# Optimization experiments

Measured on AMD Instinct MI355X. Metric: run time of the kernel, lower is better.

## Reference

```python
import jax, jax.numpy as jnp
import numpy as np

SQRT_D_K = 64 ** 0.5  # d_model ** 0.5 from __init__
NEG_INF = -1e9


def setup_inputs() -> dict:
    key = jax.random.key(0)
    kq, kk, kv, kp = jax.random.split(key, 4)
    B, H, S, Dh = 4, 16, 2048, 64
    q = jax.random.normal(kq, (B, H, S, Dh), dtype=jnp.float32)
    k = jax.random.normal(kk, (B, H, S, Dh), dtype=jnp.float32)
    v = jax.random.normal(kv, (B, H, S, Dh), dtype=jnp.float32)
    # causal mask: 1 above the diagonal (positions to mask), [1,1,S,S]
    casual_mask = jnp.triu(jnp.ones((S, S), dtype=jnp.int32), k=1)[None, None]
    # padding mask: 1 marks padded tokens, [B,S]
    padding_mask = jax.random.randint(kp, (B, S), 0, 2, dtype=jnp.int32)
    return {"q": q, "k": k, "v": v, "casual_mask": casual_mask,
            "padding_mask": padding_mask}


def reference(q, k, v, casual_mask, padding_mask):
    # score: [B,H,S,S]
    score = jnp.einsum("bhqd,bhkd->bhqk", q, k) / SQRT_D_K
    score = jnp.where(casual_mask == 1, NEG_INF, score)
    score = jnp.where(padding_mask[:, None, None, :] == 1, NEG_INF, score)
    attn_weights = jax.nn.softmax(score, axis=-1)
    # dropout p=0.0 (eval) -> identity
    attention_output = jnp.einsum("bhqk,bhkd->bhqd", attn_weights, v)
    return attention_output, attn_weights
```

## Files before the change

kernel.cpp:

```cpp
#include <hip/hip_runtime.h>
#include <hip/hip_bf16.h>

#define S_LEN 2048
#define DH    64
#define QT    128
#define KT    64
#define NW    4

typedef __attribute__((ext_vector_type(8))) short bf16x8;
typedef __attribute__((ext_vector_type(4))) float f32x4;
typedef __attribute__((ext_vector_type(4))) unsigned u32x4;
typedef __attribute__((ext_vector_type(2))) unsigned u32x2;

static __device__ __forceinline__ unsigned cvtpk(float a, float b) {
    unsigned r;
    asm("v_cvt_pk_bf16_f32 %0, %1, %2" : "=v"(r) : "v"(a), "v"(b));
    return r;
}

__global__ __launch_bounds__(256) void attn_main(
    const float* __restrict__ Q, const float* __restrict__ K,
    const float* __restrict__ V, const int* __restrict__ PAD,
    float* __restrict__ OUT, float* __restrict__ W)
{
    __shared__ short Kt[KT][72];
    __shared__ short VT[DH][72];
    __shared__ short Pb[NW][16][72];
    __shared__ float sinv[2][NW][16];
    __shared__ unsigned long long padm[32];

    const int orig = blockIdx.x;
    const int wg   = (orig & 7) * 128 + (orig >> 3);
    const int bh   = wg >> 4;
    const int qt   = 15 - (wg & 15);
    const int b    = bh >> 4;
    const int q0   = qt * QT;

    const int tid  = threadIdx.x;
    const int wv   = tid >> 6;
    const int l    = tid & 63;
    const int lr   = l & 15;
    const int lg   = l >> 4;
    const int k2   = (tid & 31) * 2;
    const int dblk = (tid >> 5) * 8;

    const size_t hoff = (size_t)bh * S_LEN * DH;
    const float* Qh = Q + hoff;
    const float* Kh = K + hoff;
    const float* Vh = V + hoff;
    float* Oh = OUT + hoff;
    float* Wh = W + (size_t)bh * S_LEN * S_LEN;

    const int nkt    = 2 * qt + 2;
    const int ktmaxA = 2 * qt;

    for (int i = tid; i < S_LEN; i += 256) {
        unsigned long long m = __ballot(PAD[b * S_LEN + i] != 0);
        if (l == 0) padm[i >> 6] = m;
    }

    bf16x8 qfA[2], qfB[2];
    #pragma unroll
    for (int blk = 0; blk < 2; ++blk) {
        const float* qp = Qh + (size_t)(q0 + blk * 64 + wv * 16 + lr) * DH + lg * 8;
        #pragma unroll
        for (int h = 0; h < 2; ++h) {
            f32x4 a  = *reinterpret_cast<const f32x4*>(qp + h * 32);
            f32x4 b4 = *reinterpret_cast<const f32x4*>(qp + h * 32 + 4);
            u32x4 t;
            t[0] = cvtpk(a[0] * 0.125f,  a[1] * 0.125f);
            t[1] = cvtpk(a[2] * 0.125f,  a[3] * 0.125f);
            t[2] = cvtpk(b4[0] * 0.125f, b4[1] * 0.125f);
            t[3] = cvtpk(b4[2] * 0.125f, b4[3] * 0.125f);
            (blk ? qfB[h] : qfA[h]) = __builtin_bit_cast(bf16x8, t);
        }
    }

    const f32x4 z4 = {0.f, 0.f, 0.f, 0.f};
    f32x4 accA[4] = {z4, z4, z4, z4};
    f32x4 accB[4] = {z4, z4, z4, z4};
    float rsA = 0.f, rsB = 0.f;
    const int qcolA = q0 + wv * 16 + lr;
    const int qcolB = qcolA + 64;

    auto ablock = [&](const bf16x8 (&qf)[2], const int qcol, float& rsref,
                      f32x4 (&accb)[4], const unsigned long long pm, const int ktbase) {
        f32x4 sc[4] = {z4, z4, z4, z4};
        #pragma unroll
        for (int s = 0; s < 4; ++s)
            #pragma unroll
            for (int h = 0; h < 2; ++h) {
                bf16x8 kf = *reinterpret_cast<const bf16x8*>(&Kt[s * 16 + lr][h * 32 + lg * 8]);
                sc[s] = __builtin_amdgcn_mfma_f32_16x16x32_bf16(kf, qf[h], sc[s], 0, 0, 0);
            }
        #pragma unroll
        for (int s = 0; s < 4; ++s) {
            const int kbase = ktbase + s * 16 + lg * 4;
            float e[4];
            #pragma unroll
            for (int r = 0; r < 4; ++r) {
                const bool padded = (pm >> (s * 16 + lg * 4 + r)) & 1ull;
                const bool ok = (kbase + r <= qcol) && !padded;
                e[r] = ok ? __expf(sc[s][r]) : 0.f;
                rsref += e[r];
            }
            u32x2 p2 = { cvtpk(e[0], e[1]), cvtpk(e[2], e[3]) };
            *reinterpret_cast<u32x2*>(&Pb[wv][lr][s * 16 + lg * 4]) = p2;
        }
        #pragma unroll
        for (int kk = 0; kk < 2; ++kk) {
            bf16x8 pf = *reinterpret_cast<const bf16x8*>(&Pb[wv][lr][kk * 32 + lg * 8]);
            #pragma unroll
            for (int dt = 0; dt < 4; ++dt) {
                bf16x8 vf = *reinterpret_cast<const bf16x8*>(&VT[dt * 16 + lr][kk * 32 + lg * 8]);
                accb[dt] = __builtin_amdgcn_mfma_f32_16x16x32_bf16(pf, vf, accb[dt], 0, 0, 0);
            }
        }
    };

    for (int kt = 0; kt < nkt; ++kt) {
        __syncthreads();
        {
            const float* kp = Kh + ((size_t)(kt * KT) + l) * DH + wv * 16;
            f32x4 pk0 = *reinterpret_cast<const f32x4*>(kp);
            f32x4 pk1 = *reinterpret_cast<const f32x4*>(kp + 4);
            f32x4 pk2 = *reinterpret_cast<const f32x4*>(kp + 8);
            f32x4 pk3 = *reinterpret_cast<const f32x4*>(kp + 12);
            const float* vp = Vh + ((size_t)(kt * KT) + k2) * DH + dblk;
            f32x4 pva0 = *reinterpret_cast<const f32x4*>(vp);
            f32x4 pva1 = *reinterpret_cast<const f32x4*>(vp + 4);
            f32x4 pvb0 = *reinterpret_cast<const f32x4*>(vp + DH);
            f32x4 pvb1 = *reinterpret_cast<const f32x4*>(vp + DH + 4);
            u32x4 ta, tb;
            ta[0] = cvtpk(pk0[0], pk0[1]); ta[1] = cvtpk(pk0[2], pk0[3]);
            ta[2] = cvtpk(pk1[0], pk1[1]); ta[3] = cvtpk(pk1[2], pk1[3]);
            tb[0] = cvtpk(pk2[0], pk2[1]); tb[1] = cvtpk(pk2[2], pk2[3]);
            tb[2] = cvtpk(pk3[0], pk3[1]); tb[3] = cvtpk(pk3[2], pk3[3]);
            *reinterpret_cast<u32x4*>(&Kt[l][wv * 16])     = ta;
            *reinterpret_cast<u32x4*>(&Kt[l][wv * 16 + 8]) = tb;
            #pragma unroll
            for (int j = 0; j < 4; ++j)
                *reinterpret_cast<unsigned*>(&VT[dblk + j][k2])     = cvtpk(pva0[j], pvb0[j]);
            #pragma unroll
            for (int j = 0; j < 4; ++j)
                *reinterpret_cast<unsigned*>(&VT[dblk + 4 + j][k2]) = cvtpk(pva1[j], pvb1[j]);
        }
        __syncthreads();

        const unsigned long long pm = padm[kt];
        if (kt <= ktmaxA) ablock(qfA, qcolA, rsA, accA, pm, kt * KT);
        ablock(qfB, qcolB, rsB, accB, pm, kt * KT);
    }

    rsA += __shfl_xor(rsA, 16, 64); rsA += __shfl_xor(rsA, 32, 64);
    rsB += __shfl_xor(rsB, 16, 64); rsB += __shfl_xor(rsB, 32, 64);
    const float invA = rsA > 0.f ? 1.f / rsA : 0.f;
    const float invB = rsB > 0.f ? 1.f / rsB : 0.f;

    if (lg == 0) { sinv[0][wv][lr] = invA; sinv[1][wv][lr] = invB; }
    float inv4A[4], inv4B[4];
    #pragma unroll
    for (int r = 0; r < 4; ++r) {
        inv4A[r] = sinv[0][wv][lg * 4 + r];
        inv4B[r] = sinv[1][wv][lg * 4 + r];
    }

    const int qa = q0 + wv * 16 + lg * 4;
    #pragma unroll
    for (int dt = 0; dt < 4; ++dt)
        #pragma unroll
        for (int r = 0; r < 4; ++r) {
            Oh[(size_t)(qa + r) * DH + dt * 16 + lr]      = accA[dt][r] * inv4A[r];
            Oh[(size_t)(qa + 64 + r) * DH + dt * 16 + lr] = accB[dt][r] * inv4B[r];
        }

    auto wblock = [&](const bf16x8 (&qf)[2], const int qcol, const float inv,
                      const unsigned long long pm, const int ktbase) {
        f32x4 sc[4] = {z4, z4, z4, z4};
        #pragma unroll
        for (int s = 0; s < 4; ++s)
            #pragma unroll
            for (int h = 0; h < 2; ++h) {
                bf16x8 kf = *reinterpret_cast<const bf16x8*>(&Kt[s * 16 + lr][h * 32 + lg * 8]);
                sc[s] = __builtin_amdgcn_mfma_f32_16x16x32_bf16(kf, qf[h], sc[s], 0, 0, 0);
            }
        #pragma unroll
        for (int s = 0; s < 4; ++s) {
            const int kbase = ktbase + s * 16 + lg * 4;
            f32x4 t;
            #pragma unroll
            for (int r = 0; r < 4; ++r) {
                const bool padded = (pm >> (s * 16 + lg * 4 + r)) & 1ull;
                const bool ok = (kbase + r <= qcol) && !padded;
                t[r] = ok ? __expf(sc[s][r]) * inv : 0.f;
            }
            __builtin_nontemporal_store(t,
                reinterpret_cast<f32x4*>(Wh + (size_t)qcol * S_LEN + kbase));
        }
    };

    for (int kt = 0; kt < nkt; ++kt) {
        __syncthreads();
        {
            const float* kp = Kh + ((size_t)(kt * KT) + l) * DH + wv * 16;
            f32x4 pk0 = *reinterpret_cast<const f32x4*>(kp);
            f32x4 pk1 = *reinterpret_cast<const f32x4*>(kp + 4);
            f32x4 pk2 = *reinterpret_cast<const f32x4*>(kp + 8);
            f32x4 pk3 = *reinterpret_cast<const f32x4*>(kp + 12);
            u32x4 ta, tb;
            ta[0] = cvtpk(pk0[0], pk0[1]); ta[1] = cvtpk(pk0[2], pk0[3]);
            ta[2] = cvtpk(pk1[0], pk1[1]); ta[3] = cvtpk(pk1[2], pk1[3]);
            tb[0] = cvtpk(pk2[0], pk2[1]); tb[1] = cvtpk(pk2[2], pk2[3]);
            tb[2] = cvtpk(pk3[0], pk3[1]); tb[3] = cvtpk(pk3[2], pk3[3]);
            *reinterpret_cast<u32x4*>(&Kt[l][wv * 16])     = ta;
            *reinterpret_cast<u32x4*>(&Kt[l][wv * 16 + 8]) = tb;
        }
        __syncthreads();

        const unsigned long long pm = padm[kt];
        if (kt <= ktmaxA) wblock(qfA, qcolA, invA, pm, kt * KT);
        wblock(qfB, qcolB, invB, pm, kt * KT);
    }

    {
        #pragma unroll 1
        for (int row = 0; row < QT; ++row) {
            const int kend = q0 + (row < 64 ? 64 : 128);
            const int n4 = (S_LEN - kend) >> 2;
            f32x4* dst = reinterpret_cast<f32x4*>(Wh + (size_t)(q0 + row) * S_LEN + kend);
            for (int i = tid; i < n4; i += 256)
                __builtin_nontemporal_store(z4, dst + i);
        }
    }
}

__global__ __launch_bounds__(256) void attn_fixup(
    const int* __restrict__ PAD, const float* __restrict__ V,
    float* __restrict__ OUT, float* __restrict__ W)
{
    const int bh = blockIdx.x;
    const int b  = bh >> 4;
    const int tid = threadIdx.x;
    __shared__ int red;
    __shared__ float tmp[256];
    __shared__ float vs[DH];
    if (tid == 0) red = S_LEN;
    __syncthreads();
    int m = S_LEN;
    for (int i = tid; i < S_LEN; i += 256)
        if (PAD[b * S_LEN + i] == 0) m = min(m, i);
    atomicMin(&red, m);
    __syncthreads();
    const int fz = red;
    if (fz == 0) return;

    const float* Vh = V + (size_t)bh * S_LEN * DH;
    float a = 0.f;
    const int dcol = tid & 63, part = tid >> 6;
    for (int kk = part; kk < S_LEN; kk += 4) a += Vh[(size_t)kk * DH + dcol];
    tmp[tid] = a;
    __syncthreads();
    if (tid < DH)
        vs[tid] = (tmp[tid] + tmp[tid + 64] + tmp[tid + 128] + tmp[tid + 192]) * (1.f / S_LEN);
    __syncthreads();

    float* Wh = W + (size_t)bh * S_LEN * S_LEN;
    float* Oh = OUT + (size_t)bh * S_LEN * DH;
    const f32x4 u = {1.f / S_LEN, 1.f / S_LEN, 1.f / S_LEN, 1.f / S_LEN};
    for (int qa2 = 0; qa2 < fz; ++qa2) {
        f32x4* dst = reinterpret_cast<f32x4*>(Wh + (size_t)qa2 * S_LEN);
        for (int i = tid; i < S_LEN / 4; i += 256) dst[i] = u;
        if (tid < DH) Oh[(size_t)qa2 * DH + tid] = vs[tid];
    }
}

extern "C" void kernel_launch(void* const* d_in, const int* in_sizes, int n_in,
                              void* d_out, int out_size, void* d_ws, size_t ws_size,
                              hipStream_t stream) {
    const float* q   = (const float*)d_in[0];
    const float* k   = (const float*)d_in[1];
    const float* v   = (const float*)d_in[2];
    const int*   pad = (const int*)d_in[4];

    float* out = (float*)d_out;
    float* w   = out + (size_t)4 * 16 * S_LEN * DH;

    attn_main<<<dim3(64 * 16), dim3(256), 0, stream>>>(q, k, v, pad, out, w);
    attn_fixup<<<dim3(64), dim3(256), 0, stream>>>(pad, v, out, w);
}
```

Baseline: 472.7 us.

## Double-buffer K tiles in LDS for the attention-weights pass with register prefetch

The weights-writing loop now prefetches the next K tile from global memory into registers before computing the current tile. After the current tile's MFMAs and stores, it converts and stores the prefetched tile into the alternate LDS buffer, reusing the VT buffer. This replaces two syncthreads per iteration with one barrier and hides global load latency behind compute. The trade-off is extra register pressure, and the code relies on VT being free and the same shape during this phase.

```diff
diff --git a/kernel.cpp b/kernel.cpp
--- a/kernel.cpp
+++ b/kernel.cpp
@@ -174,14 +174,24 @@
             Oh[(size_t)(qa + 64 + r) * DH + dt * 16 + lr] = accB[dt][r] * inv4B[r];
         }
 
-    auto wblock = [&](const bf16x8 (&qf)[2], const int qcol, const float inv,
+    auto stK = [&](short (*KB)[72], const f32x4& a0, const f32x4& a1,
+                   const f32x4& a2, const f32x4& a3) {
+        u32x4 ta, tb;
+        ta[0] = cvtpk(a0[0], a0[1]); ta[1] = cvtpk(a0[2], a0[3]);
+        ta[2] = cvtpk(a1[0], a1[1]); ta[3] = cvtpk(a1[2], a1[3]);
+        tb[0] = cvtpk(a2[0], a2[1]); tb[1] = cvtpk(a2[2], a2[3]);
+        tb[2] = cvtpk(a3[0], a3[1]); tb[3] = cvtpk(a3[2], a3[3]);
+        *reinterpret_cast<u32x4*>(&KB[l][wv * 16])     = ta;
+        *reinterpret_cast<u32x4*>(&KB[l][wv * 16 + 8]) = tb;
+    };
+    auto wblock = [&](short (*KB)[72], const bf16x8 (&qf)[2], const int qcol, const float inv,
                       const unsigned long long pm, const int ktbase) {
         f32x4 sc[4] = {z4, z4, z4, z4};
         #pragma unroll
         for (int s = 0; s < 4; ++s)
             #pragma unroll
             for (int h = 0; h < 2; ++h) {
-                bf16x8 kf = *reinterpret_cast<const bf16x8*>(&Kt[s * 16 + lr][h * 32 + lg * 8]);
+                bf16x8 kf = *reinterpret_cast<const bf16x8*>(&KB[s * 16 + lr][h * 32 + lg * 8]);
                 sc[s] = __builtin_amdgcn_mfma_f32_16x16x32_bf16(kf, qf[h], sc[s], 0, 0, 0);
             }
         #pragma unroll
@@ -199,27 +209,44 @@
         }
     };
 
+    short (*kbuf0)[72] = Kt;
+    short (*kbuf1)[72] = VT;
+
+    __syncthreads();
+    {
+        const float* kp = Kh + (size_t)l * DH + wv * 16;
+        f32x4 a0 = *reinterpret_cast<const f32x4*>(kp);
+        f32x4 a1 = *reinterpret_cast<const f32x4*>(kp + 4);
+        f32x4 a2 = *reinterpret_cast<const f32x4*>(kp + 8);
+        f32x4 a3 = *reinterpret_cast<const f32x4*>(kp + 12);
+        stK(kbuf0, a0, a1, a2, a3);
+    }
+    asm volatile("s_waitcnt lgkmcnt(0)" ::: "memory");
+    __builtin_amdgcn_sched_barrier(0);
+    __builtin_amdgcn_s_barrier();
+    __builtin_amdgcn_sched_barrier(0);
+
+    int cur = 0;
     for (int kt = 0; kt < nkt; ++kt) {
-        __syncthreads();
-        {
-            const float* kp = Kh + ((size_t)(kt * KT) + l) * DH + wv * 16;
-            f32x4 pk0 = *reinterpret_cast<const f32x4*>(kp);
-            f32x4 pk1 = *reinterpret_cast<const f32x4*>(kp + 4);
-            f32x4 pk2 = *reinterpret_cast<const f32x4*>(kp + 8);
-            f32x4 pk3 = *reinterpret_cast<const f32x4*>(kp + 12);
-            u32x4 ta, tb;
-            ta[0] = cvtpk(pk0[0], pk0[1]); ta[1] = cvtpk(pk0[2], pk0[3]);
-            ta[2] = cvtpk(pk1[0], pk1[1]); ta[3] = cvtpk(pk1[2], pk1[3]);
-            tb[0] = cvtpk(pk2[0], pk2[1]); tb[1] = cvtpk(pk2[2], pk2[3]);
-            tb[2] = cvtpk(pk3[0], pk3[1]); tb[3] = cvtpk(pk3[2], pk3[3]);
-            *reinterpret_cast<u32x4*>(&Kt[l][wv * 16])     = ta;
-            *reinterpret_cast<u32x4*>(&Kt[l][wv * 16 + 8]) = tb;
-        }
-        __syncthreads();
-
+        const bool more = (kt + 1 < nkt);
+        f32x4 n0, n1, n2, n3;
+        if (more) {
+            const float* kp = Kh + ((size_t)((kt + 1) * KT) + l) * DH + wv * 16;
+            n0 = *reinterpret_cast<const f32x4*>(kp);
+            n1 = *reinterpret_cast<const f32x4*>(kp + 4);
+            n2 = *reinterpret_cast<const f32x4*>(kp + 8);
+            n3 = *reinterpret_cast<const f32x4*>(kp + 12);
+        }
         const unsigned long long pm = padm[kt];
-        if (kt <= ktmaxA) wblock(qfA, qcolA, invA, pm, kt * KT);
-        wblock(qfB, qcolB, invB, pm, kt * KT);
+        short (*KB)[72] = cur ? kbuf1 : kbuf0;
+        if (kt <= ktmaxA) wblock(KB, qfA, qcolA, invA, pm, kt * KT);
+        wblock(KB, qfB, qcolB, invB, pm, kt * KT);
+        if (more) stK(cur ? kbuf0 : kbuf1, n0, n1, n2, n3);
+        asm volatile("s_waitcnt lgkmcnt(0)" ::: "memory");
+        __builtin_amdgcn_sched_barrier(0);
+        __builtin_amdgcn_s_barrier();
+        __builtin_amdgcn_sched_barrier(0);
+        cur ^= 1;
     }
 
     {
```

After: 488.0 us. 3.2% more time.

## Split attention-weight store pass into separate kernel with finer 64-row tiles

Applied to the files above, without the earlier changes.

The fused kernel is split in two. The first kernel computes the output and writes each row's inverse softmax sum to workspace. A second kernel uses 64-row query tiles over twice as many workgroups to recompute scores and stream out the normalized weights, and it interleaves the zero-fill of the masked upper region with the key-tile loop. This is meant to improve load balance and occupancy for the write-bound weight store and to overlap the zero-fill with compute, at the cost of an extra launch, reloading Q and K, and recomputing QK^T.

```diff
diff --git a/kernel.cpp b/kernel.cpp
--- a/kernel.cpp
+++ b/kernel.cpp
@@ -18,10 +18,10 @@
     return r;
 }
 
-__global__ __launch_bounds__(256) void attn_main(
+__global__ __launch_bounds__(256) void attn_passA(
     const float* __restrict__ Q, const float* __restrict__ K,
     const float* __restrict__ V, const int* __restrict__ PAD,
-    float* __restrict__ OUT, float* __restrict__ W)
+    float* __restrict__ OUT, float* __restrict__ INV)
 {
     __shared__ short Kt[KT][72];
     __shared__ short VT[DH][72];
@@ -49,7 +49,6 @@
     const float* Kh = K + hoff;
     const float* Vh = V + hoff;
     float* Oh = OUT + hoff;
-    float* Wh = W + (size_t)bh * S_LEN * S_LEN;
 
     const int nkt    = 2 * qt + 2;
     const int ktmaxA = 2 * qt;
@@ -157,7 +156,11 @@
     const float invA = rsA > 0.f ? 1.f / rsA : 0.f;
     const float invB = rsB > 0.f ? 1.f / rsB : 0.f;
 
-    if (lg == 0) { sinv[0][wv][lr] = invA; sinv[1][wv][lr] = invB; }
+    if (lg == 0) {
+        sinv[0][wv][lr] = invA; sinv[1][wv][lr] = invB;
+        INV[(size_t)bh * S_LEN + qcolA] = invA;
+        INV[(size_t)bh * S_LEN + qcolB] = invB;
+    }
     float inv4A[4], inv4B[4];
     #pragma unroll
     for (int r = 0; r < 4; ++r) {
@@ -173,31 +176,61 @@
             Oh[(size_t)(qa + r) * DH + dt * 16 + lr]      = accA[dt][r] * inv4A[r];
             Oh[(size_t)(qa + 64 + r) * DH + dt * 16 + lr] = accB[dt][r] * inv4B[r];
         }
-
-    auto wblock = [&](const bf16x8 (&qf)[2], const int qcol, const float inv,
-                      const unsigned long long pm, const int ktbase) {
-        f32x4 sc[4] = {z4, z4, z4, z4};
-        #pragma unroll
-        for (int s = 0; s < 4; ++s)
-            #pragma unroll
-            for (int h = 0; h < 2; ++h) {
-                bf16x8 kf = *reinterpret_cast<const bf16x8*>(&Kt[s * 16 + lr][h * 32 + lg * 8]);
-                sc[s] = __builtin_amdgcn_mfma_f32_16x16x32_bf16(kf, qf[h], sc[s], 0, 0, 0);
-            }
-        #pragma unroll
-        for (int s = 0; s < 4; ++s) {
-            const int kbase = ktbase + s * 16 + lg * 4;
-            f32x4 t;
-            #pragma unroll
-            for (int r = 0; r < 4; ++r) {
-                const bool padded = (pm >> (s * 16 + lg * 4 + r)) & 1ull;
-                const bool ok = (kbase + r <= qcol) && !padded;
-                t[r] = ok ? __expf(sc[s][r]) * inv : 0.f;
-            }
-            __builtin_nontemporal_store(t,
-                reinterpret_cast<f32x4*>(Wh + (size_t)qcol * S_LEN + kbase));
-        }
-    };
+}
+
+__global__ __launch_bounds__(256) void attn_store(
+    const float* __restrict__ Q, const float* __restrict__ K,
+    const int* __restrict__ PAD, const float* __restrict__ INV,
+    float* __restrict__ W)
+{
+    __shared__ short Kt[KT][72];
+    __shared__ unsigned long long padm[32];
+
+    const int orig = blockIdx.x;
+    const int wg   = (orig & 7) * 256 + (orig >> 3);
+    const int bh   = wg >> 5;
+    const int qt   = 31 - (wg & 31);
+    const int b    = bh >> 4;
+    const int q0   = qt * 64;
+
+    const int tid = threadIdx.x;
+    const int wv  = tid >> 6;
+    const int l   = tid & 63;
+    const int lr  = l & 15;
+    const int lg  = l >> 4;
+
+    const size_t hoff = (size_t)bh * S_LEN * DH;
+    const float* Qh = Q + hoff;
+    const float* Kh = K + hoff;
+    float* Wh = W + (size_t)bh * S_LEN * S_LEN;
+
+    const int nkt = qt + 1;
+
+    for (int i = tid; i < S_LEN; i += 256) {
+        unsigned long long m = __ballot(PAD[b * S_LEN + i] != 0);
+        if (l == 0) padm[i >> 6] = m;
+    }
+
+    bf16x8 qf[2];
+    {
+        const float* qp = Qh + (size_t)(q0 + wv * 16 + lr) * DH + lg * 8;
+        #pragma unroll
+        for (int h = 0; h < 2; ++h) {
+            f32x4 a  = *reinterpret_cast<const f32x4*>(qp + h * 32);
+            f32x4 b4 = *reinterpret_cast<const f32x4*>(qp + h * 32 + 4);
+            u32x4 t;
+            t[0] = cvtpk(a[0] * 0.125f,  a[1] * 0.125f);
+            t[1] = cvtpk(a[2] * 0.125f,  a[3] * 0.125f);
+            t[2] = cvtpk(b4[0] * 0.125f, b4[1] * 0.125f);
+            t[3] = cvtpk(b4[2] * 0.125f, b4[3] * 0.125f);
+            qf[h] = __builtin_bit_cast(bf16x8, t);
+        }
+    }
+
+    const f32x4 z4 = {0.f, 0.f, 0.f, 0.f};
+    const int qcol = q0 + wv * 16 + lr;
+    const float inv = INV[(size_t)bh * S_LEN + qcol];
+    const int rectN4 = (S_LEN - q0 - 64) >> 2;
 
     for (int kt = 0; kt < nkt; ++kt) {
         __syncthreads();
@@ -218,17 +251,32 @@
         __syncthreads();
 
         const unsigned long long pm = padm[kt];
-        if (kt <= ktmaxA) wblock(qfA, qcolA, invA, pm, kt * KT);
-        wblock(qfB, qcolB, invB, pm, kt * KT);
-    }
-
-    {
+        f32x4 sc[4] = {z4, z4, z4, z4};
+        #pragma unroll
+        for (int s = 0; s < 4; ++s)
+            #pragma unroll
+            for (int h = 0; h < 2; ++h) {
+                bf16x8 kf = *reinterpret_cast<const bf16x8*>(&Kt[s * 16 + lr][h * 32 + lg * 8]);
+                sc[s] = __builtin_amdgcn_mfma_f32_16x16x32_bf16(kf, qf[h], sc[s], 0, 0, 0);
+            }
+        #pragma unroll
+        for (int s = 0; s < 4; ++s) {
+            const int kbase = kt * KT + s * 16 + lg * 4;
+            f32x4 t;
+            #pragma unroll
+            for (int r = 0; r < 4; ++r) {
+                const bool padded = (pm >> (s * 16 + lg * 4 + r)) & 1ull;
+                const bool ok = (kbase + r <= qcol) && !padded;
+                t[r] = ok ? __expf(sc[s][r]) * inv : 0.f;
+            }
+            __builtin_nontemporal_store(t,
+                reinterpret_cast<f32x4*>(Wh + (size_t)qcol * S_LEN + kbase));
+        }
+
         #pragma unroll 1
-        for (int row = 0; row < QT; ++row) {
-            const int kend = q0 + (row < 64 ? 64 : 128);
-            const int n4 = (S_LEN - kend) >> 2;
-            f32x4* dst = reinterpret_cast<f32x4*>(Wh + (size_t)(q0 + row) * S_LEN + kend);
-            for (int i = tid; i < n4; i += 256)
+        for (int row = kt; row < 64; row += nkt) {
+            f32x4* dst = reinterpret_cast<f32x4*>(Wh + (size_t)(q0 + row) * S_LEN + q0 + 64);
+            for (int i = tid; i < rectN4; i += 256)
                 __builtin_nontemporal_store(z4, dst + i);
         }
     }
@@ -284,7 +332,9 @@
 
     float* out = (float*)d_out;
     float* w   = out + (size_t)4 * 16 * S_LEN * DH;
-
-    attn_main<<<dim3(64 * 16), dim3(256), 0, stream>>>(q, k, v, pad, out, w);
+    float* inv = (float*)d_ws;
+
+    attn_passA<<<dim3(64 * 16), dim3(256), 0, stream>>>(q, k, v, pad, out, inv);
+    attn_store<<<dim3(64 * 32), dim3(256), 0, stream>>>(q, k, pad, inv, w);
     attn_fixup<<<dim3(64), dim3(256), 0, stream>>>(pad, v, out, w);
 }
```

Result: slower. 593.0 us (+25.5%).
